# Optimization experiments

Measured on AMD Instinct MI355X. Metric: run time of the kernel, lower is better.

Reference implementation:

```python
import jax, jax.numpy as jnp
import numpy as np

B, H, W = 8, 256, 256
NF = 64          # num_feat
E = 12           # num_expert
D = NF * 4       # token dim = 256
CD = D * E       # expanded dim = 3072


def _lrelu(x):
    return jnp.where(x >= 0, x, 0.2 * x)


def _conv(x, w, stride, pad):
    return jax.lax.conv_general_dilated(
        x, w, (stride, stride), [(pad, pad), (pad, pad)],
        dimension_numbers=('NCHW', 'OIHW', 'NCHW'))


def _bn(x, g, b):
    # training-mode BatchNorm2d: batch statistics over (N, H, W)
    m = jnp.mean(x, axis=(0, 2, 3), keepdims=True)
    v = jnp.var(x, axis=(0, 2, 3), keepdims=True)
    xn = (x - m) * jax.lax.rsqrt(v + 1e-5)
    return xn * g[None, :, None, None] + b[None, :, None, None]


def setup_inputs() -> dict:
    key = jax.random.key(0)
    ks = jax.random.split(key, 16)
    s = 0.05
    d = {}
    d['x'] = jax.random.normal(ks[0], (B, 3, H, W), jnp.float32)
    d['conv0_w'] = jax.random.normal(ks[1], (NF, 3, 3, 3)) * s
    d['conv0_b'] = jnp.zeros((NF,))
    d['conv1_w'] = jax.random.normal(ks[2], (NF, NF, 4, 4)) * s
    d['bn1_g'] = jnp.ones((NF,)); d['bn1_b'] = jnp.zeros((NF,))
    d['conv2_w'] = jax.random.normal(ks[3], (2 * NF, NF, 3, 3)) * s
    d['bn2_g'] = jnp.ones((2 * NF,)); d['bn2_b'] = jnp.zeros((2 * NF,))
    d['conv3_w'] = jax.random.normal(ks[4], (2 * NF, 2 * NF, 4, 4)) * s
    d['bn3_g'] = jnp.ones((2 * NF,)); d['bn3_b'] = jnp.zeros((2 * NF,))
    d['conv4_w'] = jax.random.normal(ks[5], (4 * NF, 2 * NF, 3, 3)) * s
    d['bn4_g'] = jnp.ones((4 * NF,)); d['bn4_b'] = jnp.zeros((4 * NF,))
    d['conv5_w'] = jax.random.normal(ks[6], (4 * NF, 4 * NF, 3, 3)) * s
    d['bn5_g'] = jnp.ones((4 * NF,)); d['bn5_b'] = jnp.zeros((4 * NF,))
    d['conv6_w'] = jax.random.normal(ks[7], (4 * NF, 4 * NF, 3, 3)) * s
    d['bn6_g'] = jnp.ones((4 * NF,)); d['bn6_b'] = jnp.zeros((4 * NF,))
    d['w_gating'] = jax.random.normal(ks[8], (D, E))          # torch.randn init
    d['body_w'] = jax.random.normal(ks[9], (D, CD)) * s       # Linear(c_dim, c_dim*blocks)
    d['body_b'] = jnp.zeros((CD,))
    d['ortho_w'] = jax.random.normal(ks[10], (1, 1, CD))      # OrthorTransform weight
    d['cls_w1'] = jax.random.normal(ks[11], (D, NF // 2)) * s # shared classifier
    d['cls_b1'] = jnp.zeros((NF // 2,))
    d['cls_w2'] = jax.random.normal(ks[12], (NF // 2, 1)) * s
    d['cls_b2'] = jnp.zeros((1,))
    return d


def reference(x, conv0_w, conv0_b, conv1_w, bn1_g, bn1_b, conv2_w, bn2_g, bn2_b,
              conv3_w, bn3_g, bn3_b, conv4_w, bn4_g, bn4_b, conv5_w, bn5_g, bn5_b,
              conv6_w, bn6_g, bn6_b, w_gating, body_w, body_b, ortho_w,
              cls_w1, cls_b1, cls_w2, cls_b2):
    # --- FE conv stack ---
    h = _lrelu(_conv(x, conv0_w, 1, 1) + conv0_b[None, :, None, None])
    h = _lrelu(_bn(_conv(h, conv1_w, 2, 1), bn1_g, bn1_b))
    h = _lrelu(_bn(_conv(h, conv2_w, 1, 1), bn2_g, bn2_b))
    h = _lrelu(_bn(_conv(h, conv3_w, 2, 1), bn3_g, bn3_b))
    h = _lrelu(_bn(_conv(h, conv4_w, 1, 1), bn4_g, bn4_b))
    h = _lrelu(_bn(_conv(h, conv5_w, 1, 1), bn5_g, bn5_b))
    h = _lrelu(_bn(_conv(h, conv6_w, 1, 1), bn6_g, bn6_b))
    b, c, hh, ww = h.shape
    tok = h.reshape(b, c, hh * ww).transpose(0, 2, 1)            # (B, N, D)
    # --- softmax router ---
    routing = jax.nn.softmax(jnp.einsum('bnd,de->bne', tok, w_gating), axis=-1)
    # --- CodeReduction: Linear + lrelu, OrthorTransform multiply, lrelu ---
    feat = _lrelu(tok @ body_w + body_b)                         # (B, N, E*D)
    feat = _lrelu(feat * ortho_w)
    feat = feat.reshape(b, hh * ww, E, D)                        # torch.split chunks
    # --- shared expert MLP on every chunk (all classifiers alias one module) ---
    hid = _lrelu(jnp.einsum('bned,df->bnef', feat, cls_w1) + cls_b1)
    outs = (jnp.einsum('bnef,fo->bneo', hid, cls_w2) + cls_b2)[..., 0]  # (B,N,E)
    # --- top-1 select (equivalent to the torch.where cascade) ---
    idx = jnp.argmax(routing, axis=-1, keepdims=True)
    output = jnp.take_along_axis(outs, idx, axis=-1)             # (B, N, 1)
    return output
```

## Files before the change

kernel.cpp:

```cpp
#include <hip/hip_runtime.h>

__device__ __forceinline__ float lrelu(float x) { return x >= 0.f ? x : 0.2f * x; }

typedef const __attribute__((address_space(1))) void* gas_ptr;
typedef __attribute__((address_space(3))) void* las_ptr;

__global__ __launch_bounds__(256) void conv0_k(const float* __restrict__ x,
                                               const float* __restrict__ w,
                                               const float* __restrict__ bias,
                                               float* __restrict__ out) {
    __shared__ float sIn[3][34][34];
    __shared__ float sW[27][16];
    const int H = 256;
    int tid = threadIdx.x, tx = tid & 31, ty = tid >> 5;
    int tX = (blockIdx.x & 7) * 32, tY = (blockIdx.x >> 3) * 32;
    int b = blockIdx.y, cog = blockIdx.z * 16;
    float acc[4][16] = {};
    const float* inB = x + (size_t)b * 3 * H * H;
    for (int idx = tid; idx < 3 * 1156; idx += 256) {
        int ci = idx / 1156, r = idx % 1156, iy = r / 34, ix = r % 34;
        int gy = tY - 1 + iy, gx = tX - 1 + ix;
        float v = 0.f;
        if ((unsigned)gy < 256u && (unsigned)gx < 256u)
            v = inB[(ci * H + gy) * H + gx];
        sIn[ci][iy][ix] = v;
    }
    for (int idx = tid; idx < 27 * 16; idx += 256) {
        int co = idx & 15, rest = idx >> 4;
        sW[rest][co] = w[(cog + co) * 27 + rest];
    }
    __syncthreads();
#pragma unroll
    for (int ci = 0; ci < 3; ci++)
#pragma unroll
        for (int dy = 0; dy < 3; dy++)
#pragma unroll
            for (int dx = 0; dx < 3; dx++) {
                float a0 = sIn[ci][ty + dy][tx + dx];
                float a1 = sIn[ci][ty + 8 + dy][tx + dx];
                float a2 = sIn[ci][ty + 16 + dy][tx + dx];
                float a3 = sIn[ci][ty + 24 + dy][tx + dx];
                const float* wp = sW[ci * 9 + dy * 3 + dx];
#pragma unroll
                for (int co = 0; co < 16; co++) {
                    float wv = wp[co];
                    acc[0][co] += a0 * wv; acc[1][co] += a1 * wv;
                    acc[2][co] += a2 * wv; acc[3][co] += a3 * wv;
                }
            }
    float* outB = out + (size_t)(b * 64 + cog) * 67080;
#pragma unroll
    for (int co = 0; co < 16; co++) {
        float bv = bias[cog + co];
#pragma unroll
        for (int r = 0; r < 4; r++)
            outB[(size_t)co * 67080 + (size_t)(tY + ty + 8 * r + 1) * 260 +
                 tX + tx + 1] = lrelu(acc[r][co] + bv);
    }
}

template <int COG>
__device__ __forceinline__ void stats_epilogue(float (&acc)[4][COG], float* red,
                                               double2* part, int cog,
                                               int slotBase, int S, int tid) {
#pragma unroll
    for (int c = 0; c < COG; c++) {
        float s = 0.f, q = 0.f;
#pragma unroll
        for (int j = 0; j < 4; j++) { float v = acc[j][c]; s += v; q += v * v; }
        red[c * 256 + tid] = s;
        red[COG * 256 + c * 256 + tid] = q;
    }
    __syncthreads();
    for (int off = 128; off; off >>= 1) {
        if (tid < off) {
#pragma unroll
            for (int c = 0; c < COG; c++) {
                red[c * 256 + tid] += red[c * 256 + tid + off];
                red[COG * 256 + c * 256 + tid] +=
                    red[COG * 256 + c * 256 + tid + off];
            }
        }
        __syncthreads();
    }
    if (tid < COG) {
        int slot = slotBase + blockIdx.y * gridDim.x + blockIdx.x;
        part[(size_t)(cog + tid) * S + slot].x = (double)red[tid * 256];
        part[(size_t)(cog + tid) * S + slot].y =
            (double)red[COG * 256 + tid * 256];
    }
}

template <int COG>
__global__ __launch_bounds__(256) void c4x4p_k(const float* __restrict__ in,
                                               const float* __restrict__ w,
                                               float* __restrict__ out,
                                               double2* __restrict__ part,
                                               int slotBase, int S,
                                               int Cin, int Cout, int Hin,
                                               int Hp, int Wp,
                                               int oHp, int oWp, int oOff) {
    __shared__ float sIn[2][4488];
    __shared__ float sW[2][16 * COG];
    const int Hout = Hin >> 1;
    const int tid = threadIdx.x, tx = tid & 31, ty = tid >> 5;
    const int tpr = Hout >> 5;
    const int tX = (blockIdx.x % tpr) * 32, tY = (blockIdx.x / tpr) * 32;
    const int b = blockIdx.y, cog = blockIdx.z * COG;
    const int HWin = Hp * Wp;
    const float* inB = in + (size_t)b * Cin * HWin;
    const int wvbase = tid & ~63;

    int gOff[5]; int lOff[5]; bool act[5];
#pragma unroll
    for (int r = 0; r < 5; r++) {
        int idx = tid + r * 256;
        bool a = idx < 1122;
        int row = idx / 17, c4 = idx % 17;
        gOff[r] = a ? ((2 * tY + row) * Wp + 2 * tX + 4 * c4) : 0;
        lOff[r] = (r * 256 + wvbase) * 4;
        act[r] = a;
    }
    const int wco = tid % COG, wt = tid / COG;
    const int wgo = ((cog + wco) * Cin) * 16 + wt;
    const bool wact = tid < 16 * COG;

    float acc[4][COG];
#pragma unroll
    for (int j = 0; j < 4; j++)
#pragma unroll
        for (int c = 0; c < COG; c++) acc[j][c] = 0.f;

#pragma unroll
    for (int r = 0; r < 5; r++)
        if (act[r])
            __builtin_amdgcn_global_load_lds((gas_ptr)(inB + gOff[r]),
                                             (las_ptr)(&sIn[0][lOff[r]]), 16, 0, 0);
    if (wact)
        __builtin_amdgcn_global_load_lds((gas_ptr)(w + wgo),
                                         (las_ptr)(&sW[0][wvbase]), 4, 0, 0);
    __syncthreads();

    for (int k = 0; k < Cin; k++) {
        const int cur = k & 1, nb = cur ^ 1;
        const bool more = (k + 1) < Cin;
        if (more) {
            const float* p = inB + (size_t)(k + 1) * HWin;
#pragma unroll
            for (int r = 0; r < 5; r++)
                if (act[r])
                    __builtin_amdgcn_global_load_lds(
                        (gas_ptr)(p + gOff[r]),
                        (las_ptr)(&sIn[nb][lOff[r]]), 16, 0, 0);
            if (wact)
                __builtin_amdgcn_global_load_lds(
                    (gas_ptr)(w + wgo + (k + 1) * 16),
                    (las_ptr)(&sW[nb][wvbase]), 4, 0, 0);
        }
        const float* sI = sIn[cur];
        const float* sw = sW[cur];
#pragma unroll
        for (int dy = 0; dy < 4; dy++)
#pragma unroll
            for (int dx = 0; dx < 4; dx++) {
                const float* bp = sI + (2 * ty + dy) * 68 + 2 * tx + dx;
                float a0 = bp[0];
                float a1 = bp[16 * 68];
                float a2 = bp[32 * 68];
                float a3 = bp[48 * 68];
                const float* wp = sw + (dy * 4 + dx) * COG;
#pragma unroll
                for (int c = 0; c < COG; c++) {
                    float wv = wp[c];
                    acc[0][c] += a0 * wv; acc[1][c] += a1 * wv;
                    acc[2][c] += a2 * wv; acc[3][c] += a3 * wv;
                }
            }
        __syncthreads();
    }

    float* outB = out + (size_t)(b * Cout + cog) * oHp * oWp;
#pragma unroll
    for (int c = 0; c < COG; c++)
#pragma unroll
        for (int r = 0; r < 4; r++)
            outB[(size_t)c * oHp * oWp +
                 (size_t)(tY + ty + 8 * r + oOff) * oWp + tX + tx + oOff] =
                acc[r][c];
    stats_epilogue<COG>(acc, &sIn[0][0], part, cog, slotBase, S, tid);
}

template <int COG>
__global__ __launch_bounds__(256) void c3x3_k(const float* __restrict__ in,
                                              const float* __restrict__ w,
                                              float* __restrict__ out,
                                              double2* __restrict__ part,
                                              int slotBase, int S,
                                              int Cin, int Cout, int H,
                                              int Hp, int Wp,
                                              int oHp, int oWp, int oOff) {
    constexpr int RS = 36;
    constexpr int CI = 34 * RS;
    __shared__ float sIn[2][2 * CI];
    __shared__ float sW[2][18 * COG];
    const int tid = threadIdx.x, tx = tid & 31, ty = tid >> 5;
    const int tpr = H >> 5;
    const int tX = (blockIdx.x % tpr) * 32, tY = (blockIdx.x / tpr) * 32;
    const int b = blockIdx.y, cog = blockIdx.z * COG;
    const int HWin = Hp * Wp;
    const float* inB = in + (size_t)b * Cin * HWin;
    const int wvbase = tid & ~63;

    int gOff[3]; int lOff[3]; bool act[3];
#pragma unroll
    for (int r = 0; r < 3; r++) {
        int idx = tid + r * 256;
        bool a = idx < 612;
        int ci = idx / 306, rem = idx % 306;
        int row = rem / 9, c4 = rem % 9;
        gOff[r] = a ? (ci * HWin + (tY + row) * Wp + tX + 4 * c4) : 0;
        lOff[r] = (r * 256 + wvbase) * 4;
        act[r] = a;
    }
    constexpr int NW = (18 * COG + 255) / 256;
    int wgo[NW]; bool wact[NW];
#pragma unroll
    for (int r = 0; r < NW; r++) {
        int widx = tid + r * 256;
        bool a = widx < 18 * COG;
        int co = widx % COG, rest = widx / COG;
        int ci = rest / 9, t = rest % 9;
        wgo[r] = a ? (((cog + co) * Cin + ci) * 9 + t) : 0;
        wact[r] = a;
    }

    float acc[4][COG];
#pragma unroll
    for (int j = 0; j < 4; j++)
#pragma unroll
        for (int c = 0; c < COG; c++) acc[j][c] = 0.f;

    const int steps = Cin >> 1;

#pragma unroll
    for (int r = 0; r < 3; r++)
        if (act[r])
            __builtin_amdgcn_global_load_lds(
                (gas_ptr)(inB + gOff[r]),
                (las_ptr)(&sIn[0][lOff[r]]), 16, 0, 0);
#pragma unroll
    for (int r = 0; r < NW; r++)
        if (wact[r])
            __builtin_amdgcn_global_load_lds(
                (gas_ptr)(w + wgo[r]),
                (las_ptr)(&sW[0][r * 256 + wvbase]), 4, 0, 0);
    __syncthreads();

    for (int k = 0; k < steps; k++) {
        const int cur = k & 1;
        const int nb = cur ^ 1;
        const bool more = (k + 1) < steps;
        if (more) {
            const int c0n = 2 * (k + 1);
            const float* p = inB + (size_t)c0n * HWin;
            const float* wp2 = w + (size_t)c0n * 9;
#pragma unroll
            for (int r = 0; r < 3; r++)
                if (act[r])
                    __builtin_amdgcn_global_load_lds(
                        (gas_ptr)(p + gOff[r]),
                        (las_ptr)(&sIn[nb][lOff[r]]), 16, 0, 0);
#pragma unroll
            for (int r = 0; r < NW; r++)
                if (wact[r])
                    __builtin_amdgcn_global_load_lds(
                        (gas_ptr)(wp2 + wgo[r]),
                        (las_ptr)(&sW[nb][r * 256 + wvbase]), 4, 0, 0);
        }
        const float* sI = sIn[cur];
        const float* sw = sW[cur];
#pragma unroll
        for (int ci = 0; ci < 2; ci++)
#pragma unroll
            for (int dx = 0; dx < 3; dx++) {
                const float* bp = sI + ci * CI + (4 * ty) * RS + tx + dx;
                float a[6];
#pragma unroll
                for (int j = 0; j < 6; j++) a[j] = bp[j * RS];
#pragma unroll
                for (int dy = 0; dy < 3; dy++) {
                    const float* wp = sw + (ci * 9 + dy * 3 + dx) * COG;
#pragma unroll
                    for (int c = 0; c < COG; c++) {
                        float wv = wp[c];
                        acc[0][c] += a[0 + dy] * wv;
                        acc[1][c] += a[1 + dy] * wv;
                        acc[2][c] += a[2 + dy] * wv;
                        acc[3][c] += a[3 + dy] * wv;
                    }
                }
            }
        __syncthreads();
    }

    float* outB = out + (size_t)(b * Cout + cog) * oHp * oWp;
#pragma unroll
    for (int c = 0; c < COG; c++)
#pragma unroll
        for (int j = 0; j < 4; j++)
            outB[(size_t)c * oHp * oWp +
                 (size_t)(tY + 4 * ty + j + oOff) * oWp + tX + tx + oOff] =
                acc[j][c];
    stats_epilogue<COG>(acc, &sIn[0][0], part, cog, slotBase, S, tid);
}

__global__ void bnfin_k(const double2* __restrict__ part, int S, int C, double invN,
                        const float* __restrict__ g, const float* __restrict__ bb,
                        float2* __restrict__ ss) {
    int c = threadIdx.x;
    if (c >= C) return;
    double sum = 0.0, sq = 0.0;
    for (int s = 0; s < S; s++) {
        double2 p = part[(size_t)c * S + s];
        sum += p.x; sq += p.y;
    }
    double m = sum * invN;
    double v = sq * invN - m * m;
    double sc = (double)g[c] / sqrt(v + 1e-5);
    ss[c] = make_float2((float)sc, (float)((double)bb[c] - m * sc));
}

__global__ __launch_bounds__(256) void bnact_k(float* __restrict__ p,
                                               const float2* __restrict__ ss,
                                               int C, int H, int W,
                                               int Hp, int Wp) {
    int pc = blockIdx.x;
    int c = pc & (C - 1);
    float2 t = ss ? ss[c] : make_float2(1.f, 0.f);
    bool xf = (ss != nullptr);
    float* pl = p + (size_t)pc * Hp * Wp;
    int n = Hp * Wp;
    for (int i = threadIdx.x; i < n; i += 256) {
        int y = i / Wp, x = i - y * Wp;
        bool inter = (y >= 1) && (y <= H) && (x >= 1) && (x <= W);
        if (!inter) pl[i] = 0.f;
        else if (xf) { float v = pl[i]; pl[i] = lrelu(t.x * v + t.y); }
    }
}

__global__ __launch_bounds__(256) void transp_k(const float* __restrict__ h6,
                                                const float2* __restrict__ ss,
                                                float* __restrict__ tok) {
    __shared__ float sT[32][33];
    int tx = threadIdx.x & 31, ty = threadIdx.x >> 5;
    int n0 = blockIdx.x * 32, d0 = blockIdx.y * 32, b = blockIdx.z;
    const float* hb = h6 + ((size_t)b * 256 + d0) * 4096 + n0;
#pragma unroll
    for (int r = 0; r < 4; r++) {
        int d = ty + 8 * r;
        float2 t = ss[d0 + d];
        sT[d][tx] = lrelu(t.x * hb[d * 4096 + tx] + t.y);
    }
    __syncthreads();
    float* tb = tok + ((size_t)b * 4096 + n0) * 256 + d0;
#pragma unroll
    for (int r = 0; r < 4; r++) {
        int n = ty + 8 * r;
        tb[n * 256 + tx] = sT[tx][n];
    }
}

__global__ __launch_bounds__(256) void token_k(const float* __restrict__ tok,
                                               const float* __restrict__ wg,
                                               const float* __restrict__ bw,
                                               const float* __restrict__ bb,
                                               const float* __restrict__ ow,
                                               const float* __restrict__ w1,
                                               const float* __restrict__ b1,
                                               const float* __restrict__ w2,
                                               const float* __restrict__ b2,
                                               float* __restrict__ outp) {
    __shared__ float sf[4][256];
    const int tid = threadIdx.x, wave = tid >> 6, l = tid & 63;
    const int t = blockIdx.x * 4 + wave;
    const float4 tv = reinterpret_cast<const float4*>(tok + (size_t)t * 256)[l];
    sf[wave][4 * l + 0] = tv.x; sf[wave][4 * l + 1] = tv.y;
    sf[wave][4 * l + 2] = tv.z; sf[wave][4 * l + 3] = tv.w;

    float lg[12];
#pragma unroll
    for (int e = 0; e < 12; e++) lg[e] = 0.f;
    const float tj[4] = {tv.x, tv.y, tv.z, tv.w};
#pragma unroll
    for (int j = 0; j < 4; j++) {
        const float* wr = wg + (4 * l + j) * 12;
#pragma unroll
        for (int e = 0; e < 12; e++) lg[e] += tj[j] * wr[e];
    }
#pragma unroll
    for (int off = 32; off > 0; off >>= 1) {
#pragma unroll
        for (int e = 0; e < 12; e++) lg[e] += __shfl_xor(lg[e], off);
    }
    int idx = 0; float best = lg[0];
#pragma unroll
    for (int e = 1; e < 12; e++)
        if (lg[e] > best) { best = lg[e]; idx = e; }
    const int cb = idx * 256;

    float f0 = 0.f, f1 = 0.f, f2 = 0.f, f3 = 0.f;
    const float* bwp = bw + cb + 4 * l;
#pragma unroll 4
    for (int d = 0; d < 256; d++) {
        const float td = sf[wave][d];
        const float4 wv = *reinterpret_cast<const float4*>(bwp + (size_t)d * 3072);
        f0 += td * wv.x; f1 += td * wv.y;
        f2 += td * wv.z; f3 += td * wv.w;
    }
    float fj[4] = {f0, f1, f2, f3};
#pragma unroll
    for (int j = 0; j < 4; j++) {
        int jj = cb + 4 * l + j;
        float v = lrelu(fj[j] + bb[jj]);
        v = lrelu(v * ow[jj]);
        sf[wave][4 * l + j] = v;
    }

    float o = 0.f;
    if (l < 32) {
        float h = b1[l];
#pragma unroll 4
        for (int j = 0; j < 256; j++) h += sf[wave][j] * w1[j * 32 + l];
        h = lrelu(h);
        o = h * w2[l];
    }
    o += __shfl_xor(o, 16); o += __shfl_xor(o, 8); o += __shfl_xor(o, 4);
    o += __shfl_xor(o, 2);  o += __shfl_xor(o, 1);
    if (l == 0) outp[t] = o + b2[0];
}

extern "C" void kernel_launch(void* const* d_in, const int* in_sizes, int n_in,
                              void* d_out, int out_size, void* d_ws, size_t ws_size,
                              hipStream_t stream) {
    const float* x   = (const float*)d_in[0];
    const float* w0  = (const float*)d_in[1];
    const float* b0  = (const float*)d_in[2];
    const float* w1  = (const float*)d_in[3];
    const float* g1  = (const float*)d_in[4];
    const float* be1 = (const float*)d_in[5];
    const float* w2  = (const float*)d_in[6];
    const float* g2  = (const float*)d_in[7];
    const float* be2 = (const float*)d_in[8];
    const float* w3  = (const float*)d_in[9];
    const float* g3  = (const float*)d_in[10];
    const float* be3 = (const float*)d_in[11];
    const float* w4  = (const float*)d_in[12];
    const float* g4  = (const float*)d_in[13];
    const float* be4 = (const float*)d_in[14];
    const float* w5  = (const float*)d_in[15];
    const float* g5  = (const float*)d_in[16];
    const float* be5 = (const float*)d_in[17];
    const float* w6  = (const float*)d_in[18];
    const float* g6  = (const float*)d_in[19];
    const float* be6 = (const float*)d_in[20];
    const float* wg  = (const float*)d_in[21];
    const float* bw  = (const float*)d_in[22];
    const float* bbp = (const float*)d_in[23];
    const float* owp = (const float*)d_in[24];
    const float* cw1 = (const float*)d_in[25];
    const float* cb1 = (const float*)d_in[26];
    const float* cw2 = (const float*)d_in[27];
    const float* cb2 = (const float*)d_in[28];

    char* W = (char*)d_ws;
    float2* ssb = (float2*)W;
    float2* ss1 = ssb;
    float2* ss2 = ssb + 64;
    float2* ss3 = ssb + 192;
    float2* ss4 = ssb + 320;
    float2* ss5 = ssb + 576;
    float2* ss6 = ssb + 832;
    double2* part = (double2*)(W + 16384);

    char* BIG = W + 278528;
    float* h0p = (float*)(BIG);
    float* h1p = (float*)(BIG + 70287360);
    float* h2p = (float*)(BIG);
    float* h3p = (float*)(BIG + 70287360);
    float* h4p = (float*)(BIG);
    float* h5p = (float*)(BIG + 36765696);
    float* h6  = (float*)(BIG);
    float* tok = (float*)(BIG + 36765696);

    bnact_k<<<256, 256, 0, stream>>>(h0p, nullptr, 64, 256, 256, 258, 260);
    for (int half = 0; half < 2; half++) {
        conv0_k<<<dim3(64, 4, 4), 256, 0, stream>>>(
            x + (size_t)half * 4 * 3 * 65536, w0, b0, h0p);
        c4x4p_k<8><<<dim3(16, 4, 8), 256, 0, stream>>>(
            h0p, w1, h1p + (size_t)half * 4 * 64 * 17160, part, half * 64, 128,
            64, 64, 256, 258, 260, 130, 132, 1);
    }
    bnfin_k<<<1, 256, 0, stream>>>(part, 128, 64, 1.0 / 131072.0, g1, be1, ss1);
    bnact_k<<<512, 256, 0, stream>>>(h1p, ss1, 64, 128, 128, 130, 132);
    c3x3_k<8><<<dim3(16, 8, 16), 256, 0, stream>>>(
        h1p, w2, h2p, part, 0, 128, 64, 128, 128, 130, 132, 130, 132, 1);
    bnfin_k<<<1, 256, 0, stream>>>(part, 128, 128, 1.0 / 131072.0, g2, be2, ss2);
    bnact_k<<<1024, 256, 0, stream>>>(h2p, ss2, 128, 128, 128, 130, 132);
    c4x4p_k<8><<<dim3(4, 8, 16), 256, 0, stream>>>(
        h2p, w3, h3p, part, 0, 32, 128, 128, 128, 130, 132, 66, 68, 1);
    bnfin_k<<<1, 256, 0, stream>>>(part, 32, 128, 1.0 / 32768.0, g3, be3, ss3);
    bnact_k<<<1024, 256, 0, stream>>>(h3p, ss3, 128, 64, 64, 66, 68);
    c3x3_k<8><<<dim3(4, 8, 32), 256, 0, stream>>>(
        h3p, w4, h4p, part, 0, 32, 128, 256, 64, 66, 68, 66, 68, 1);
    bnfin_k<<<1, 256, 0, stream>>>(part, 32, 256, 1.0 / 32768.0, g4, be4, ss4);
    bnact_k<<<2048, 256, 0, stream>>>(h4p, ss4, 256, 64, 64, 66, 68);
    c3x3_k<8><<<dim3(4, 8, 32), 256, 0, stream>>>(
        h4p, w5, h5p, part, 0, 32, 256, 256, 64, 66, 68, 66, 68, 1);
    bnfin_k<<<1, 256, 0, stream>>>(part, 32, 256, 1.0 / 32768.0, g5, be5, ss5);
    bnact_k<<<2048, 256, 0, stream>>>(h5p, ss5, 256, 64, 64, 66, 68);
    c3x3_k<8><<<dim3(4, 8, 32), 256, 0, stream>>>(
        h5p, w6, h6, part, 0, 32, 256, 256, 64, 66, 68, 64, 64, 0);
    bnfin_k<<<1, 256, 0, stream>>>(part, 32, 256, 1.0 / 32768.0, g6, be6, ss6);
    transp_k<<<dim3(128, 8, 8), 256, 0, stream>>>(h6, ss6, tok);
    token_k<<<8192, 256, 0, stream>>>(tok, wg, bw, bbp, owp, cw1, cb1, cw2, cb2,
                                      (float*)d_out);
}
```

Before: 2.628 ms.

## Double c3x3 output tile height and use wave-shuffle BN stats reduction

The 3x3 conv kernel now computes a 32x64 output tile per block, with 8 rows per thread instead of 4. This improves input-halo reuse and raises FMA work per shared-memory load. Grid sizes and partial-stat slot counts are halved to match. The BN statistics epilogue now reduces with wave shuffles and a small per-wave shared buffer instead of a 256-wide shared-memory tree with repeated barriers. In exchange the kernel uses more registers and shared memory (about 38KB for the input buffers) and launches fewer blocks, which may reduce occupancy and latency hiding.

```diff
diff --git a/kernel.cpp b/kernel.cpp
--- a/kernel.cpp
+++ b/kernel.cpp
@@ -59,35 +59,39 @@
     }
 }
 
-template <int COG>
-__device__ __forceinline__ void stats_epilogue(float (&acc)[4][COG], float* red,
-                                               double2* part, int cog,
-                                               int slotBase, int S, int tid) {
+template <int COG, int RPT>
+__device__ __forceinline__ void stats_epi(float (&acc)[RPT][COG], float2* sRed,
+                                          double2* part, int cog, int slotBase,
+                                          int S, int tid) {
+    const int lane = tid & 63, wv = tid >> 6;
+    float s[COG], q[COG];
 #pragma unroll
     for (int c = 0; c < COG; c++) {
-        float s = 0.f, q = 0.f;
-#pragma unroll
-        for (int j = 0; j < 4; j++) { float v = acc[j][c]; s += v; q += v * v; }
-        red[c * 256 + tid] = s;
-        red[COG * 256 + c * 256 + tid] = q;
-    }
+        float ss = 0.f, qq = 0.f;
+#pragma unroll
+        for (int j = 0; j < RPT; j++) { float v = acc[j][c]; ss += v; qq += v * v; }
+        s[c] = ss; q[c] = qq;
+    }
+#pragma unroll
+    for (int off = 32; off; off >>= 1)
+#pragma unroll
+        for (int c = 0; c < COG; c++) {
+            s[c] += __shfl_xor(s[c], off);
+            q[c] += __shfl_xor(q[c], off);
+        }
+    if (lane == 0)
+#pragma unroll
+        for (int c = 0; c < COG; c++) sRed[wv * COG + c] = make_float2(s[c], q[c]);
     __syncthreads();
-    for (int off = 128; off; off >>= 1) {
-        if (tid < off) {
-#pragma unroll
-            for (int c = 0; c < COG; c++) {
-                red[c * 256 + tid] += red[c * 256 + tid + off];
-                red[COG * 256 + c * 256 + tid] +=
-                    red[COG * 256 + c * 256 + tid + off];
-            }
+    if (tid < COG) {
+        double ss = 0.0, qq = 0.0;
+#pragma unroll
+        for (int wvi = 0; wvi < 4; wvi++) {
+            float2 p = sRed[wvi * COG + tid];
+            ss += (double)p.x; qq += (double)p.y;
         }
-        __syncthreads();
-    }
-    if (tid < COG) {
         int slot = slotBase + blockIdx.y * gridDim.x + blockIdx.x;
-        part[(size_t)(cog + tid) * S + slot].x = (double)red[tid * 256];
-        part[(size_t)(cog + tid) * S + slot].y =
-            (double)red[COG * 256 + tid * 256];
+        part[(size_t)(cog + tid) * S + slot] = make_double2(ss, qq);
     }
 }
 
@@ -102,6 +106,7 @@
                                                int oHp, int oWp, int oOff) {
     __shared__ float sIn[2][4488];
     __shared__ float sW[2][16 * COG];
+    __shared__ float2 sRed[4 * COG];
     const int Hout = Hin >> 1;
     const int tid = threadIdx.x, tx = tid & 31, ty = tid >> 5;
     const int tpr = Hout >> 5;
@@ -187,7 +192,7 @@
             outB[(size_t)c * oHp * oWp +
                  (size_t)(tY + ty + 8 * r + oOff) * oWp + tX + tx + oOff] =
                 acc[r][c];
-    stats_epilogue<COG>(acc, &sIn[0][0], part, cog, slotBase, S, tid);
+    stats_epi<COG, 4>(acc, sRed, part, cog, slotBase, S, tid);
 }
 
 template <int COG>
@@ -200,60 +205,57 @@
                                               int Hp, int Wp,
                                               int oHp, int oWp, int oOff) {
     constexpr int RS = 36;
-    constexpr int CI = 34 * RS;
+    constexpr int ROWS = 66;
+    constexpr int CI = ROWS * RS;
+    constexpr int NSF4 = 2 * ROWS * 9;
+    constexpr int NR = 5;
     __shared__ float sIn[2][2 * CI];
     __shared__ float sW[2][18 * COG];
+    __shared__ float2 sRed[4 * COG];
     const int tid = threadIdx.x, tx = tid & 31, ty = tid >> 5;
     const int tpr = H >> 5;
-    const int tX = (blockIdx.x % tpr) * 32, tY = (blockIdx.x / tpr) * 32;
+    const int tX = (blockIdx.x % tpr) * 32, tY = (blockIdx.x / tpr) * 64;
     const int b = blockIdx.y, cog = blockIdx.z * COG;
     const int HWin = Hp * Wp;
     const float* inB = in + (size_t)b * Cin * HWin;
     const int wvbase = tid & ~63;
 
-    int gOff[3]; int lOff[3]; bool act[3];
-#pragma unroll
-    for (int r = 0; r < 3; r++) {
+    int gOff[NR]; int lOff[NR]; bool act[NR];
+#pragma unroll
+    for (int r = 0; r < NR; r++) {
         int idx = tid + r * 256;
-        bool a = idx < 612;
-        int ci = idx / 306, rem = idx % 306;
+        bool a = idx < NSF4;
+        int ci = idx / (9 * ROWS), rem = idx % (9 * ROWS);
         int row = rem / 9, c4 = rem % 9;
         gOff[r] = a ? (ci * HWin + (tY + row) * Wp + tX + 4 * c4) : 0;
         lOff[r] = (r * 256 + wvbase) * 4;
         act[r] = a;
     }
-    constexpr int NW = (18 * COG + 255) / 256;
-    int wgo[NW]; bool wact[NW];
-#pragma unroll
-    for (int r = 0; r < NW; r++) {
-        int widx = tid + r * 256;
-        bool a = widx < 18 * COG;
-        int co = widx % COG, rest = widx / COG;
+    const bool wact = tid < 18 * COG;
+    int wgo;
+    {
+        int co = tid % COG, rest = tid / COG;
         int ci = rest / 9, t = rest % 9;
-        wgo[r] = a ? (((cog + co) * Cin + ci) * 9 + t) : 0;
-        wact[r] = a;
-    }
-
-    float acc[4][COG];
-#pragma unroll
-    for (int j = 0; j < 4; j++)
+        wgo = ((cog + co) * Cin + ci) * 9 + t;
+    }
+
+    float acc[8][COG];
+#pragma unroll
+    for (int j = 0; j < 8; j++)
 #pragma unroll
         for (int c = 0; c < COG; c++) acc[j][c] = 0.f;
 
     const int steps = Cin >> 1;
 
 #pragma unroll
-    for (int r = 0; r < 3; r++)
+    for (int r = 0; r < NR; r++)
         if (act[r])
             __builtin_amdgcn_global_load_lds(
                 (gas_ptr)(inB + gOff[r]),
                 (las_ptr)(&sIn[0][lOff[r]]), 16, 0, 0);
-#pragma unroll
-    for (int r = 0; r < NW; r++)
-        if (wact[r])
-            __builtin_amdgcn_global_load_lds(
-                (gas_ptr)(w + wgo[r]),
-                (las_ptr)(&sW[0][r * 256 + wvbase]), 4, 0, 0);
+    if (wact)
+        __builtin_amdgcn_global_load_lds((gas_ptr)(w + wgo),
+                                         (las_ptr)(&sW[0][wvbase]), 4, 0, 0);
     __syncthreads();
 
     for (int k = 0; k < steps; k++) {
@@ -263,19 +265,16 @@
         if (more) {
             const int c0n = 2 * (k + 1);
             const float* p = inB + (size_t)c0n * HWin;
-            const float* wp2 = w + (size_t)c0n * 9;
-#pragma unroll
-            for (int r = 0; r < 3; r++)
+#pragma unroll
+            for (int r = 0; r < NR; r++)
                 if (act[r])
                     __builtin_amdgcn_global_load_lds(
                         (gas_ptr)(p + gOff[r]),
                         (las_ptr)(&sIn[nb][lOff[r]]), 16, 0, 0);
-#pragma unroll
-            for (int r = 0; r < NW; r++)
-                if (wact[r])
-                    __builtin_amdgcn_global_load_lds(
-                        (gas_ptr)(wp2 + wgo[r]),
-                        (las_ptr)(&sW[nb][r * 256 + wvbase]), 4, 0, 0);
+            if (wact)
+                __builtin_amdgcn_global_load_lds(
+                    (gas_ptr)(w + (size_t)c0n * 9 + wgo),
+                    (las_ptr)(&sW[nb][wvbase]), 4, 0, 0);
         }
         const float* sI = sIn[cur];
         const float* sw = sW[cur];
@@ -283,20 +282,19 @@
         for (int ci = 0; ci < 2; ci++)
 #pragma unroll
             for (int dx = 0; dx < 3; dx++) {
-                const float* bp = sI + ci * CI + (4 * ty) * RS + tx + dx;
-                float a[6];
-#pragma unroll
-                for (int j = 0; j < 6; j++) a[j] = bp[j * RS];
+                const float* bp = sI + ci * CI + (8 * ty) * RS + tx + dx;
+                float a[10];
+#pragma unroll
+                for (int j = 0; j < 10; j++) a[j] = bp[j * RS];
 #pragma unroll
                 for (int dy = 0; dy < 3; dy++) {
                     const float* wp = sw + (ci * 9 + dy * 3 + dx) * COG;
 #pragma unroll
                     for (int c = 0; c < COG; c++) {
                         float wv = wp[c];
-                        acc[0][c] += a[0 + dy] * wv;
-                        acc[1][c] += a[1 + dy] * wv;
-                        acc[2][c] += a[2 + dy] * wv;
-                        acc[3][c] += a[3 + dy] * wv;
+#pragma unroll
+                        for (int j = 0; j < 8; j++)
+                            acc[j][c] += a[j + dy] * wv;
                     }
                 }
             }
@@ -307,11 +305,11 @@
 #pragma unroll
     for (int c = 0; c < COG; c++)
 #pragma unroll
-        for (int j = 0; j < 4; j++)
+        for (int j = 0; j < 8; j++)
             outB[(size_t)c * oHp * oWp +
-                 (size_t)(tY + 4 * ty + j + oOff) * oWp + tX + tx + oOff] =
+                 (size_t)(tY + 8 * ty + j + oOff) * oWp + tX + tx + oOff] =
                 acc[j][c];
-    stats_epilogue<COG>(acc, &sIn[0][0], part, cog, slotBase, S, tid);
+    stats_epi<COG, 8>(acc, sRed, part, cog, slotBase, S, tid);
 }
 
 __global__ void bnfin_k(const double2* __restrict__ part, int S, int C, double invN,
@@ -502,25 +500,25 @@
     }
     bnfin_k<<<1, 256, 0, stream>>>(part, 128, 64, 1.0 / 131072.0, g1, be1, ss1);
     bnact_k<<<512, 256, 0, stream>>>(h1p, ss1, 64, 128, 128, 130, 132);
-    c3x3_k<8><<<dim3(16, 8, 16), 256, 0, stream>>>(
-        h1p, w2, h2p, part, 0, 128, 64, 128, 128, 130, 132, 130, 132, 1);
-    bnfin_k<<<1, 256, 0, stream>>>(part, 128, 128, 1.0 / 131072.0, g2, be2, ss2);
+    c3x3_k<8><<<dim3(8, 8, 16), 256, 0, stream>>>(
+        h1p, w2, h2p, part, 0, 64, 64, 128, 128, 130, 132, 130, 132, 1);
+    bnfin_k<<<1, 256, 0, stream>>>(part, 64, 128, 1.0 / 131072.0, g2, be2, ss2);
     bnact_k<<<1024, 256, 0, stream>>>(h2p, ss2, 128, 128, 128, 130, 132);
     c4x4p_k<8><<<dim3(4, 8, 16), 256, 0, stream>>>(
         h2p, w3, h3p, part, 0, 32, 128, 128, 128, 130, 132, 66, 68, 1);
     bnfin_k<<<1, 256, 0, stream>>>(part, 32, 128, 1.0 / 32768.0, g3, be3, ss3);
     bnact_k<<<1024, 256, 0, stream>>>(h3p, ss3, 128, 64, 64, 66, 68);
-    c3x3_k<8><<<dim3(4, 8, 32), 256, 0, stream>>>(
-        h3p, w4, h4p, part, 0, 32, 128, 256, 64, 66, 68, 66, 68, 1);
-    bnfin_k<<<1, 256, 0, stream>>>(part, 32, 256, 1.0 / 32768.0, g4, be4, ss4);
+    c3x3_k<8><<<dim3(2, 8, 32), 256, 0, stream>>>(
+        h3p, w4, h4p, part, 0, 16, 128, 256, 64, 66, 68, 66, 68, 1);
+    bnfin_k<<<1, 256, 0, stream>>>(part, 16, 256, 1.0 / 32768.0, g4, be4, ss4);
     bnact_k<<<2048, 256, 0, stream>>>(h4p, ss4, 256, 64, 64, 66, 68);
-    c3x3_k<8><<<dim3(4, 8, 32), 256, 0, stream>>>(
-        h4p, w5, h5p, part, 0, 32, 256, 256, 64, 66, 68, 66, 68, 1);
-    bnfin_k<<<1, 256, 0, stream>>>(part, 32, 256, 1.0 / 32768.0, g5, be5, ss5);
+    c3x3_k<8><<<dim3(2, 8, 32), 256, 0, stream>>>(
+        h4p, w5, h5p, part, 0, 16, 256, 256, 64, 66, 68, 66, 68, 1);
+    bnfin_k<<<1, 256, 0, stream>>>(part, 16, 256, 1.0 / 32768.0, g5, be5, ss5);
     bnact_k<<<2048, 256, 0, stream>>>(h5p, ss5, 256, 64, 64, 66, 68);
-    c3x3_k<8><<<dim3(4, 8, 32), 256, 0, stream>>>(
-        h5p, w6, h6, part, 0, 32, 256, 256, 64, 66, 68, 64, 64, 0);
-    bnfin_k<<<1, 256, 0, stream>>>(part, 32, 256, 1.0 / 32768.0, g6, be6, ss6);
+    c3x3_k<8><<<dim3(2, 8, 32), 256, 0, stream>>>(
+        h5p, w6, h6, part, 0, 16, 256, 256, 64, 66, 68, 64, 64, 0);
+    bnfin_k<<<1, 256, 0, stream>>>(part, 16, 256, 1.0 / 32768.0, g6, be6, ss6);
     transp_k<<<dim3(128, 8, 8), 256, 0, stream>>>(h6, ss6, tok);
     token_k<<<8192, 256, 0, stream>>>(tok, wg, bw, bbp, owp, cw1, cb1, cw2, cb2,
                                       (float*)d_out);
```

Result: faster. 2.568 ms (-2.3%).
